# Kernel tuning notes

Hardware: AMD Instinct MI355X
Metric: run time of the kernel (lower is better)

Reference implementation:

```python
import jax, jax.numpy as jnp
import numpy as np

N = 100_000
E = 1_000_000
F_IN = 128
F_OUT = 64
NHOP = 2


def _xavier(k, shape, gain=1.414):
    fan_in, fan_out = shape
    std = gain * np.sqrt(2.0 / (fan_in + fan_out))
    return (jax.random.normal(k, shape) * std).astype(jnp.float32)


def setup_inputs() -> dict:
    key = jax.random.key(0)
    ks = jax.random.split(key, 8)
    x = jax.random.normal(ks[0], (N, F_IN), jnp.float32)
    edge_index = jax.random.randint(ks[1], (2, E), 0, N)
    edge_attr = jax.random.uniform(ks[2], (E,), jnp.float32)
    W0 = _xavier(ks[3], (F_IN, F_OUT))
    W1 = _xavier(ks[4], (F_IN, F_OUT))
    b0 = jnp.zeros((F_OUT,), jnp.float32)
    b1 = jnp.zeros((F_OUT,), jnp.float32)
    fc0 = _xavier(ks[5], (F_OUT, 1))
    fc1 = _xavier(ks[6], (F_OUT, 1))
    bf0 = jnp.zeros((1,), jnp.float32)
    bf1 = jnp.zeros((1,), jnp.float32)
    return dict(x=x, edge_index=edge_index, edge_attr=edge_attr,
                W0=W0, b0=b0, W1=W1, b1=b1,
                fc0=fc0, bf0=bf0, fc1=fc1, bf1=bf1)


def _spmm(row, col, val, v, n):
    # (A v)[r] = sum over edges (r -> c) of val * v[c]
    return jax.ops.segment_sum(val[:, None] * v[col], row, num_segments=n)


def _adaptive_enc(y, fc, bf):
    # NodeAdaptiveEncoder (eval mode): relu(y) + sigmoid(y@fc+bf) * min(y, 0)
    g = jax.nn.sigmoid(y @ fc + bf)  # [N, 1]
    return jnp.where(y < 0, 0.0, y) + g * jnp.where(y > 0, 0.0, y)


def reference(x, edge_index, edge_attr, W0, b0, W1, b1, fc0, bf0, fc1, bf1):
    n = x.shape[0]
    row, col = edge_index[0], edge_index[1]
    ones = jnp.ones((n, 1), x.dtype)
    params = [(W0, b0, fc0, bf0), (W1, b1, fc1, bf1)]
    outs = []
    for hop in range(NHOP):
        W, b, fc, bf = params[hop]
        h = x @ W  # [N, F_OUT]
        # identity attention; row_uniform norm of A^(hop+1) factors as
        # (A^(hop+1) h) / (A^(hop+1) 1) -- exact since spspmm sums duplicates.
        agg, deg = h, ones
        for _ in range(hop + 1):
            agg = _spmm(row, col, edge_attr, agg, n)
            deg = _spmm(row, col, edge_attr, deg, n)
        safe_deg = jnp.where(deg > 0, deg, 1.0)
        y = jnp.where(deg > 0, agg / safe_deg, 0.0)  # NaN mask for empty rows
        y = y + b
        outs.append(_adaptive_enc(y, fc, bf))
    return jnp.concatenate(outs, axis=1)  # [N, NHOP * F_OUT]
```

## Files before the change

kernel.cpp:

```cpp
#include <hip/hip_runtime.h>

#define F_IN 128
#define F_ALL 128
#define F_HOP 64

#define RPB_BITS 9
#define RPB 512
#define KB_MAX 256
#define NBLK_BIN 256
#define BCAP 16

typedef unsigned int uint;
typedef unsigned short ushort;
typedef __attribute__((ext_vector_type(8))) short short8v;
typedef __attribute__((ext_vector_type(4))) float float4v;

__device__ __forceinline__ uint pack_bf16(float lo, float hi) {
    uint ul = __float_as_uint(lo), uh = __float_as_uint(hi);
    ul += 0x7FFFu + ((ul >> 16) & 1u);
    uh += 0x7FFFu + ((uh >> 16) & 1u);
    return (ul >> 16) | (uh & 0xFFFF0000u);
}
__device__ __forceinline__ float bf_lo(uint h) { return __uint_as_float(h << 16); }
__device__ __forceinline__ float bf_hi(uint h) { return __uint_as_float(h & 0xFFFF0000u); }
__device__ __forceinline__ ushort to_bf16(float x) {
    uint u = __float_as_uint(x);
    u += 0x7FFFu + ((u >> 16) & 1u);
    return (ushort)(u >> 16);
}

__global__ __launch_bounds__(256) void gemm_mfma_kernel(
    const float* __restrict__ x, const float* __restrict__ W0,
    const float* __restrict__ W1, uint* __restrict__ H2, int N) {
    __shared__ ushort Wlds[16384];

    {
        const int t = threadIdx.x;
        #pragma unroll
        for (int i = 0; i < 8; ++i) {
            const int e    = t + 256 * i;
            const int lane = e & 63;
            const int tile = e >> 6;
            const int kt   = tile >> 3;
            const int nt   = tile & 7;
            const int k0   = kt * 32 + (lane >> 4) * 8;
            const int n    = nt * 16 + (lane & 15);
            const float* src = (n < 64) ? (W0 + n) : (W1 + (n - 64));
            float v[8];
            #pragma unroll
            for (int j = 0; j < 8; ++j) v[j] = src[(size_t)(k0 + j) * F_HOP];
            uint4 o;
            o.x = pack_bf16(v[0], v[1]);
            o.y = pack_bf16(v[2], v[3]);
            o.z = pack_bf16(v[4], v[5]);
            o.w = pack_bf16(v[6], v[7]);
            *((uint4*)Wlds + e) = o;
        }
    }
    __syncthreads();

    const int wv   = threadIdx.x >> 6;
    const int lane = threadIdx.x & 63;
    const int rbase = blockIdx.x * 64 + wv * 16;
    if (rbase >= N) return;

    const int m    = lane & 15;
    const int quad = lane >> 4;
    const float* xrow = x + (size_t)(rbase + m) * F_IN + quad * 8;

    float4v acc[8];
    #pragma unroll
    for (int t = 0; t < 8; ++t) acc[t] = (float4v){0.f, 0.f, 0.f, 0.f};

    #pragma unroll
    for (int kt = 0; kt < 4; ++kt) {
        const float4 xa = *(const float4*)(xrow + kt * 32);
        const float4 xb = *(const float4*)(xrow + kt * 32 + 4);
        union { uint4 u; short8v s; } av;
        av.u.x = pack_bf16(xa.x, xa.y);
        av.u.y = pack_bf16(xa.z, xa.w);
        av.u.z = pack_bf16(xb.x, xb.y);
        av.u.w = pack_bf16(xb.z, xb.w);
        #pragma unroll
        for (int nt = 0; nt < 8; ++nt) {
            union { uint4 u; short8v s; } bv;
            bv.u = *((const uint4*)Wlds + (kt * 8 + nt) * 64 + lane);
            acc[nt] = __builtin_amdgcn_mfma_f32_16x16x32_bf16(av.s, bv.s, acc[nt], 0, 0, 0);
        }
    }

    #pragma unroll
    for (int t = 0; t < 4; ++t) {
        #pragma unroll
        for (int i = 0; i < 4; ++i) {
            const int r = rbase + quad * 4 + i;
            H2[(size_t)r * F_HOP + t * 16 + m] = pack_bf16(acc[t][i], acc[t + 4][i]);
        }
    }
}

__global__ __launch_bounds__(256) void bucket_hist_kernel(
    const int* __restrict__ ei, int* __restrict__ bhist, int E, int K) {
    __shared__ int h[KB_MAX];
    for (int i = threadIdx.x; i < K; i += 256) h[i] = 0;
    __syncthreads();
    const int chunk = (E + NBLK_BIN - 1) / NBLK_BIN;
    const int s = blockIdx.x * chunk;
    const int e = min(s + chunk, E);
    for (int j = s + threadIdx.x; j < e; j += 256)
        atomicAdd(&h[ei[j] >> RPB_BITS], 1);
    __syncthreads();
    for (int i = threadIdx.x; i < K; i += 256)
        bhist[blockIdx.x * KB_MAX + i] = h[i];
}

__global__ __launch_bounds__(256) void bucket_scan_kernel(
    int* __restrict__ bhist, int* __restrict__ bbase,
    int* __restrict__ rowptr, int E, int K, int N) {
    __shared__ int wsum[4];
    const int t = threadIdx.x;
    int s = 0;
    if (t < K)
        for (int i = 0; i < NBLK_BIN; ++i) s += bhist[i * KB_MAX + t];
    int v = s;
    #pragma unroll
    for (int d = 1; d < 64; d <<= 1) {
        int u = __shfl_up(v, (unsigned)d, 64);
        if ((t & 63) >= d) v += u;
    }
    if ((t & 63) == 63) wsum[t >> 6] = v;
    __syncthreads();
    int off = 0;
    #pragma unroll
    for (int i = 0; i < 4; ++i) if (i < (t >> 6)) off += wsum[i];
    const int excl = off + v - s;
    if (t < K) {
        bbase[t] = excl;
        int run = excl;
        for (int i = 0; i < NBLK_BIN; ++i) {
            const int idx = i * KB_MAX + t;
            const int c = bhist[idx];
            bhist[idx] = run;
            run += c;
        }
    }
    if (t == 0) { bbase[K] = E; rowptr[N] = E; }
}

__global__ __launch_bounds__(256) void bin_kernel(
    const int* __restrict__ ei, const float* __restrict__ ea,
    const int* __restrict__ bloc, int2* __restrict__ gbuf, int E, int K) {
    __shared__ int buf[KB_MAX * (2 * BCAP + 1)];
    __shared__ int lcnt[KB_MAX];
    __shared__ int cur[KB_MAX];
    for (int i = threadIdx.x; i < K; i += 256) {
        lcnt[i] = 0;
        cur[i] = bloc[blockIdx.x * KB_MAX + i];
    }
    __syncthreads();
    const int chunk = (E + NBLK_BIN - 1) / NBLK_BIN;
    const int s0 = blockIdx.x * chunk;
    const int e0 = min(s0 + chunk, E);
    for (int base = s0; base < e0; base += 256) {
        const int j = base + threadIdx.x;
        if (j < e0) {
            const int r = ei[j];
            const int c = ei[E + j];
            const int vv = __float_as_int(ea[j]);
            const int b = r >> RPB_BITS;
            const int w0 = c | ((r & (RPB - 1)) << 17);
            const int pos = atomicAdd(&lcnt[b], 1);
            if (pos < BCAP) {
                const int boff = b * (2 * BCAP + 1) + 2 * pos;
                buf[boff] = w0; buf[boff + 1] = vv;
            } else {
                const int gp = atomicAdd(&cur[b], 1);
                gbuf[gp] = make_int2(w0, vv);
            }
        }
        __syncthreads();
        for (int b = threadIdx.x; b < K; b += 256) {
            int c = lcnt[b]; if (c > BCAP) c = BCAP;
            if (c >= 8) {
                const int n = c & ~7;
                const int gp = cur[b]; cur[b] = gp + n;
                const int boff = b * (2 * BCAP + 1);
                for (int i = 0; i < n; ++i)
                    gbuf[gp + i] = make_int2(buf[boff + 2 * i], buf[boff + 2 * i + 1]);
                for (int i = n; i < c; ++i) {
                    buf[boff + 2 * (i - n)]     = buf[boff + 2 * i];
                    buf[boff + 2 * (i - n) + 1] = buf[boff + 2 * i + 1];
                }
                lcnt[b] = c - n;
            } else {
                lcnt[b] = c;
            }
        }
        __syncthreads();
    }
    for (int b = threadIdx.x; b < K; b += 256) {
        int c = lcnt[b]; if (c > BCAP) c = BCAP;
        if (c > 0) {
            const int gp = cur[b];
            const int boff = b * (2 * BCAP + 1);
            for (int i = 0; i < c; ++i)
                gbuf[gp + i] = make_int2(buf[boff + 2 * i], buf[boff + 2 * i + 1]);
        }
    }
}

__global__ __launch_bounds__(256) void sort_kernel(
    const int* __restrict__ bbase, const int2* __restrict__ gbuf,
    int2* __restrict__ ecv, int* __restrict__ rowptr, int N) {
    __shared__ int cnt[RPB];
    __shared__ int nxt[RPB];
    __shared__ int wsum[4];
    const int b = blockIdx.x;
    const int t = threadIdx.x;
    const int bstart = bbase[b], bend = bbase[b + 1];
    const int row0 = b << RPB_BITS;
    for (int i = t; i < RPB; i += 256) cnt[i] = 0;
    __syncthreads();
    for (int j = bstart + t; j < bend; j += 256)
        atomicAdd(&cnt[(gbuf[j].x >> 17) & (RPB - 1)], 1);
    __syncthreads();
    const int c0 = cnt[2 * t], c1 = cnt[2 * t + 1];
    const int s = c0 + c1;
    int v = s;
    #pragma unroll
    for (int d = 1; d < 64; d <<= 1) {
        int u = __shfl_up(v, (unsigned)d, 64);
        if ((t & 63) >= d) v += u;
    }
    if ((t & 63) == 63) wsum[t >> 6] = v;
    __syncthreads();
    int off = 0;
    #pragma unroll
    for (int i = 0; i < 4; ++i) if (i < (t >> 6)) off += wsum[i];
    const int e0 = off + v - s;
    nxt[2 * t]     = e0;
    nxt[2 * t + 1] = e0 + c0;
    const int r0 = row0 + 2 * t, r1 = row0 + 2 * t + 1;
    if (r0 < N) rowptr[r0] = bstart + e0;
    if (r1 < N) rowptr[r1] = bstart + e0 + c0;
    __syncthreads();
    for (int j = bstart + t; j < bend; j += 256) {
        const int2 p = gbuf[j];
        const int lr = (p.x >> 17) & (RPB - 1);
        const int pos = atomicAdd(&nxt[lr], 1);
        ecv[bstart + pos] = make_int2(p.x & 0x1FFFF, p.y);
    }
}

__global__ __launch_bounds__(256) void pass1_kernel(
    const int* __restrict__ rowptr, const int2* __restrict__ ecv,
    const uint* __restrict__ H2,
    const float* __restrict__ b0, const float* __restrict__ fc0,
    const float* __restrict__ bf0,
    float* __restrict__ out, ushort* __restrict__ T16,
    float* __restrict__ dg1, int N) {
    const int lane = threadIdx.x & 63;
    const int g    = lane >> 4;
    const int l    = lane & 15;
    const int r = blockIdx.x * 16 + (threadIdx.x >> 6) * 4 + g;
    if (r >= N) return;
    const int f0 = l * 4;
    const uint* __restrict__ H2b = H2 + f0;
    const int jb = rowptr[r], je = rowptr[r + 1];

    float s00 = 0.f, s01 = 0.f, s02 = 0.f, s03 = 0.f;
    float s10 = 0.f, s11 = 0.f, s12 = 0.f, s13 = 0.f;
    float d = 0.f;
    int j = jb;
    for (; j + 4 <= je; j += 4) {
        const int2 e0 = ecv[j], e1 = ecv[j + 1], e2 = ecv[j + 2], e3 = ecv[j + 3];
        const uint4 h0 = *(const uint4*)(H2b + (size_t)e0.x * F_HOP);
        const uint4 h1 = *(const uint4*)(H2b + (size_t)e1.x * F_HOP);
        const uint4 h2 = *(const uint4*)(H2b + (size_t)e2.x * F_HOP);
        const uint4 h3 = *(const uint4*)(H2b + (size_t)e3.x * F_HOP);
        const float v0 = __int_as_float(e0.y), v1 = __int_as_float(e1.y);
        const float v2 = __int_as_float(e2.y), v3 = __int_as_float(e3.y);
        d += (v0 + v1) + (v2 + v3);
        s00 = fmaf(v0, bf_lo(h0.x), s00); s10 = fmaf(v0, bf_hi(h0.x), s10);
        s01 = fmaf(v0, bf_lo(h0.y), s01); s11 = fmaf(v0, bf_hi(h0.y), s11);
        s02 = fmaf(v0, bf_lo(h0.z), s02); s12 = fmaf(v0, bf_hi(h0.z), s12);
        s03 = fmaf(v0, bf_lo(h0.w), s03); s13 = fmaf(v0, bf_hi(h0.w), s13);
        s00 = fmaf(v1, bf_lo(h1.x), s00); s10 = fmaf(v1, bf_hi(h1.x), s10);
        s01 = fmaf(v1, bf_lo(h1.y), s01); s11 = fmaf(v1, bf_hi(h1.y), s11);
        s02 = fmaf(v1, bf_lo(h1.z), s02); s12 = fmaf(v1, bf_hi(h1.z), s12);
        s03 = fmaf(v1, bf_lo(h1.w), s03); s13 = fmaf(v1, bf_hi(h1.w), s13);
        s00 = fmaf(v2, bf_lo(h2.x), s00); s10 = fmaf(v2, bf_hi(h2.x), s10);
        s01 = fmaf(v2, bf_lo(h2.y), s01); s11 = fmaf(v2, bf_hi(h2.y), s11);
        s02 = fmaf(v2, bf_lo(h2.z), s02); s12 = fmaf(v2, bf_hi(h2.z), s12);
        s03 = fmaf(v2, bf_lo(h2.w), s03); s13 = fmaf(v2, bf_hi(h2.w), s13);
        s00 = fmaf(v3, bf_lo(h3.x), s00); s10 = fmaf(v3, bf_hi(h3.x), s10);
        s01 = fmaf(v3, bf_lo(h3.y), s01); s11 = fmaf(v3, bf_hi(h3.y), s11);
        s02 = fmaf(v3, bf_lo(h3.z), s02); s12 = fmaf(v3, bf_hi(h3.z), s12);
        s03 = fmaf(v3, bf_lo(h3.w), s03); s13 = fmaf(v3, bf_hi(h3.w), s13);
    }
    for (; j < je; ++j) {
        const int2 e0 = ecv[j];
        const uint4 h0 = *(const uint4*)(H2b + (size_t)e0.x * F_HOP);
        const float v0 = __int_as_float(e0.y);
        d += v0;
        s00 = fmaf(v0, bf_lo(h0.x), s00); s10 = fmaf(v0, bf_hi(h0.x), s10);
        s01 = fmaf(v0, bf_lo(h0.y), s01); s11 = fmaf(v0, bf_hi(h0.y), s11);
        s02 = fmaf(v0, bf_lo(h0.z), s02); s12 = fmaf(v0, bf_hi(h0.z), s12);
        s03 = fmaf(v0, bf_lo(h0.w), s03); s13 = fmaf(v0, bf_hi(h0.w), s13);
    }

    uint2 tw;
    tw.x = pack_bf16(s10, s11);
    tw.y = pack_bf16(s12, s13);
    *(uint2*)(T16 + (size_t)r * F_HOP + f0) = tw;
    if (l == 0) dg1[r] = d;

    const float inv = (d > 0.f) ? 1.f / d : 0.f;
    const float4 bb = *(const float4*)(b0 + f0);
    const float4 ff = *(const float4*)(fc0 + f0);
    const float y0 = s00 * inv + bb.x;
    const float y1 = s01 * inv + bb.y;
    const float y2 = s02 * inv + bb.z;
    const float y3 = s03 * inv + bb.w;
    float t = y0 * ff.x + y1 * ff.y + y2 * ff.z + y3 * ff.w;
    #pragma unroll
    for (int m = 1; m < 16; m <<= 1) t += __shfl_xor(t, m, 64);
    const float gg = 1.f / (1.f + __expf(-(t + bf0[0])));
    float4 o;
    o.x = fmaxf(y0, 0.f) + gg * fminf(y0, 0.f);
    o.y = fmaxf(y1, 0.f) + gg * fminf(y1, 0.f);
    o.z = fmaxf(y2, 0.f) + gg * fminf(y2, 0.f);
    o.w = fmaxf(y3, 0.f) + gg * fminf(y3, 0.f);
    *(float4*)(out + (size_t)r * F_ALL + f0) = o;
}

__global__ __launch_bounds__(256) void pass2_kernel(
    const int* __restrict__ rowptr, const int2* __restrict__ ecv,
    const ushort* __restrict__ T16, const float* __restrict__ dg1,
    const float* __restrict__ b1, const float* __restrict__ fc1,
    const float* __restrict__ bf1,
    float* __restrict__ out, int N) {
    const int lane = threadIdx.x & 63;
    const int g    = lane >> 4;
    const int l    = lane & 15;
    const int r = blockIdx.x * 16 + (threadIdx.x >> 6) * 4 + g;
    if (r >= N) return;
    const int f0 = l * 4;
    const ushort* __restrict__ Tb = T16 + f0;
    const int jb = rowptr[r], je = rowptr[r + 1];

    float s0 = 0.f, s1 = 0.f, s2 = 0.f, s3 = 0.f;
    float d2 = 0.f;
    int j = jb;
    for (; j + 4 <= je; j += 4) {
        const int2 e0 = ecv[j], e1 = ecv[j + 1], e2 = ecv[j + 2], e3 = ecv[j + 3];
        const uint2 t0 = *(const uint2*)(Tb + (size_t)e0.x * F_HOP);
        const uint2 t1 = *(const uint2*)(Tb + (size_t)e1.x * F_HOP);
        const uint2 t2 = *(const uint2*)(Tb + (size_t)e2.x * F_HOP);
        const uint2 t3 = *(const uint2*)(Tb + (size_t)e3.x * F_HOP);
        const float g0 = dg1[e0.x], g1 = dg1[e1.x], g2 = dg1[e2.x], g3 = dg1[e3.x];
        const float v0 = __int_as_float(e0.y), v1 = __int_as_float(e1.y);
        const float v2 = __int_as_float(e2.y), v3 = __int_as_float(e3.y);
        d2 = fmaf(v0, g0, d2); d2 = fmaf(v1, g1, d2);
        d2 = fmaf(v2, g2, d2); d2 = fmaf(v3, g3, d2);
        s0 = fmaf(v0, bf_lo(t0.x), s0); s1 = fmaf(v0, bf_hi(t0.x), s1);
        s2 = fmaf(v0, bf_lo(t0.y), s2); s3 = fmaf(v0, bf_hi(t0.y), s3);
        s0 = fmaf(v1, bf_lo(t1.x), s0); s1 = fmaf(v1, bf_hi(t1.x), s1);
        s2 = fmaf(v1, bf_lo(t1.y), s2); s3 = fmaf(v1, bf_hi(t1.y), s3);
        s0 = fmaf(v2, bf_lo(t2.x), s0); s1 = fmaf(v2, bf_hi(t2.x), s1);
        s2 = fmaf(v2, bf_lo(t2.y), s2); s3 = fmaf(v2, bf_hi(t2.y), s3);
        s0 = fmaf(v3, bf_lo(t3.x), s0); s1 = fmaf(v3, bf_hi(t3.x), s1);
        s2 = fmaf(v3, bf_lo(t3.y), s2); s3 = fmaf(v3, bf_hi(t3.y), s3);
    }
    for (; j < je; ++j) {
        const int2 e0 = ecv[j];
        const uint2 t0 = *(const uint2*)(Tb + (size_t)e0.x * F_HOP);
        const float v0 = __int_as_float(e0.y);
        d2 = fmaf(v0, dg1[e0.x], d2);
        s0 = fmaf(v0, bf_lo(t0.x), s0); s1 = fmaf(v0, bf_hi(t0.x), s1);
        s2 = fmaf(v0, bf_lo(t0.y), s2); s3 = fmaf(v0, bf_hi(t0.y), s3);
    }

    const float inv = (d2 > 0.f) ? 1.f / d2 : 0.f;
    const float4 bb = *(const float4*)(b1 + f0);
    const float4 ff = *(const float4*)(fc1 + f0);
    const float y0 = s0 * inv + bb.x;
    const float y1 = s1 * inv + bb.y;
    const float y2 = s2 * inv + bb.z;
    const float y3 = s3 * inv + bb.w;
    float t = y0 * ff.x + y1 * ff.y + y2 * ff.z + y3 * ff.w;
    #pragma unroll
    for (int m = 1; m < 16; m <<= 1) t += __shfl_xor(t, m, 64);
    const float gg = 1.f / (1.f + __expf(-(t + bf1[0])));
    float4 o;
    o.x = fmaxf(y0, 0.f) + gg * fminf(y0, 0.f);
    o.y = fmaxf(y1, 0.f) + gg * fminf(y1, 0.f);
    o.z = fmaxf(y2, 0.f) + gg * fminf(y2, 0.f);
    o.w = fmaxf(y3, 0.f) + gg * fminf(y3, 0.f);
    *(float4*)(out + (size_t)r * F_ALL + F_HOP + f0) = o;
}

extern "C" void kernel_launch(void* const* d_in, const int* in_sizes, int n_in,
                              void* d_out, int out_size, void* d_ws, size_t ws_size,
                              hipStream_t stream) {
    const float* x   = (const float*)d_in[0];
    const int*   ei  = (const int*)  d_in[1];
    const float* ea  = (const float*)d_in[2];
    const float* W0  = (const float*)d_in[3];
    const float* b0  = (const float*)d_in[4];
    const float* W1  = (const float*)d_in[5];
    const float* b1  = (const float*)d_in[6];
    const float* fc0 = (const float*)d_in[7];
    const float* bf0 = (const float*)d_in[8];
    const float* fc1 = (const float*)d_in[9];
    const float* bf1 = (const float*)d_in[10];
    float* out = (float*)d_out;

    const int N = in_sizes[0] / F_IN;
    const int E = in_sizes[2];
    const int K = (N + RPB - 1) >> RPB_BITS;

    uint*   H2   = (uint*)d_ws;
    ushort* T16  = (ushort*)(H2 + (size_t)N * F_HOP);
    float*  dg1  = (float*)(T16 + (size_t)N * F_HOP);
    int2*   gbuf = (int2*)(dg1 + (size_t)((N + 3) & ~3));
    int2*   ecv  = gbuf + (size_t)E;
    int*    bhist = (int*)(ecv + (size_t)E);
    int*    bbase = bhist + (size_t)NBLK_BIN * KB_MAX;
    int*    rowptr = bbase + (KB_MAX + 8);

    gemm_mfma_kernel<<<(N + 63) / 64, 256, 0, stream>>>(x, W0, W1, H2, N);

    bucket_hist_kernel<<<NBLK_BIN, 256, 0, stream>>>(ei, bhist, E, K);
    bucket_scan_kernel<<<1, 256, 0, stream>>>(bhist, bbase, rowptr, E, K, N);
    bin_kernel<<<NBLK_BIN, 256, 0, stream>>>(ei, ea, bhist, gbuf, E, K);
    sort_kernel<<<K, 256, 0, stream>>>(bbase, gbuf, ecv, rowptr, N);

    pass1_kernel<<<(N + 15) / 16, 256, 0, stream>>>(
        rowptr, ecv, H2, b0, fc0, bf0, out, T16, dg1, N);

    pass2_kernel<<<(N + 15) / 16, 256, 0, stream>>>(
        rowptr, ecv, T16, dg1, b1, fc1, bf1, out, N);
}
```

Measured before the change: 258.3 us.

## Parallelize bucket scan, simplify binning, stage bucket edges in LDS during sort

Replaces the single-block serial bucket scan with a per-bucket parallel block scan followed by a small total scan. The binning kernel drops its LDS staging buffers and writes each edge straight to global memory via a shared-memory cursor atomic. The sort kernel now runs 512 threads, one per row in the bucket, and caches up to ECAP edges in LDS so the second pass avoids re-reading global memory. This targets the serial scan latency and the heavy synchronisation in binning, at the cost of less coalesced scatter writes and a large LDS footprint in sort that may limit occupancy.

After: 235.5 us. 1.1x faster.

```diff
diff --git a/kernel.cpp b/kernel.cpp
--- a/kernel.cpp
+++ b/kernel.cpp
@@ -8,7 +8,7 @@
 #define RPB 512
 #define KB_MAX 256
 #define NBLK_BIN 256
-#define BCAP 16
+#define ECAP 6144
 
 typedef unsigned int uint;
 typedef unsigned short ushort;
@@ -23,11 +23,6 @@
 }
 __device__ __forceinline__ float bf_lo(uint h) { return __uint_as_float(h << 16); }
 __device__ __forceinline__ float bf_hi(uint h) { return __uint_as_float(h & 0xFFFF0000u); }
-__device__ __forceinline__ ushort to_bf16(float x) {
-    uint u = __float_as_uint(x);
-    u += 0x7FFFu + ((u >> 16) & 1u);
-    return (ushort)(u >> 16);
-}
 
 __global__ __launch_bounds__(256) void gemm_mfma_kernel(
     const float* __restrict__ x, const float* __restrict__ W0,
@@ -114,14 +109,33 @@
         bhist[blockIdx.x * KB_MAX + i] = h[i];
 }
 
-__global__ __launch_bounds__(256) void bucket_scan_kernel(
-    int* __restrict__ bhist, int* __restrict__ bbase,
+__global__ __launch_bounds__(256) void blockscan_kernel(
+    int* __restrict__ bhist, int* __restrict__ btot) {
+    __shared__ int wsum[4];
+    const int b = blockIdx.x;
+    const int t = threadIdx.x;
+    const int s = bhist[t * KB_MAX + b];
+    int v = s;
+    #pragma unroll
+    for (int d = 1; d < 64; d <<= 1) {
+        int u = __shfl_up(v, (unsigned)d, 64);
+        if ((t & 63) >= d) v += u;
+    }
+    if ((t & 63) == 63) wsum[t >> 6] = v;
+    __syncthreads();
+    int off = 0;
+    #pragma unroll
+    for (int i = 0; i < 4; ++i) if (i < (t >> 6)) off += wsum[i];
+    bhist[t * KB_MAX + b] = off + v - s;
+    if (t == 255) btot[b] = off + v;
+}
+
+__global__ __launch_bounds__(256) void total_scan_kernel(
+    const int* __restrict__ btot, int* __restrict__ bbase,
     int* __restrict__ rowptr, int E, int K, int N) {
     __shared__ int wsum[4];
     const int t = threadIdx.x;
-    int s = 0;
-    if (t < K)
-        for (int i = 0; i < NBLK_BIN; ++i) s += bhist[i * KB_MAX + t];
+    const int s = (t < K) ? btot[t] : 0;
     int v = s;
     #pragma unroll
     for (int d = 1; d < 64; d <<= 1) {
@@ -134,98 +148,51 @@
     #pragma unroll
     for (int i = 0; i < 4; ++i) if (i < (t >> 6)) off += wsum[i];
     const int excl = off + v - s;
-    if (t < K) {
-        bbase[t] = excl;
-        int run = excl;
-        for (int i = 0; i < NBLK_BIN; ++i) {
-            const int idx = i * KB_MAX + t;
-            const int c = bhist[idx];
-            bhist[idx] = run;
-            run += c;
-        }
-    }
+    if (t < K) bbase[t] = excl;
     if (t == 0) { bbase[K] = E; rowptr[N] = E; }
 }
 
 __global__ __launch_bounds__(256) void bin_kernel(
     const int* __restrict__ ei, const float* __restrict__ ea,
-    const int* __restrict__ bloc, int2* __restrict__ gbuf, int E, int K) {
-    __shared__ int buf[KB_MAX * (2 * BCAP + 1)];
-    __shared__ int lcnt[KB_MAX];
+    const int* __restrict__ bloc, const int* __restrict__ bbase,
+    int2* __restrict__ gbuf, int E, int K) {
     __shared__ int cur[KB_MAX];
-    for (int i = threadIdx.x; i < K; i += 256) {
-        lcnt[i] = 0;
-        cur[i] = bloc[blockIdx.x * KB_MAX + i];
-    }
+    for (int i = threadIdx.x; i < K; i += 256)
+        cur[i] = bbase[i] + bloc[blockIdx.x * KB_MAX + i];
     __syncthreads();
     const int chunk = (E + NBLK_BIN - 1) / NBLK_BIN;
     const int s0 = blockIdx.x * chunk;
     const int e0 = min(s0 + chunk, E);
-    for (int base = s0; base < e0; base += 256) {
-        const int j = base + threadIdx.x;
-        if (j < e0) {
-            const int r = ei[j];
-            const int c = ei[E + j];
-            const int vv = __float_as_int(ea[j]);
-            const int b = r >> RPB_BITS;
-            const int w0 = c | ((r & (RPB - 1)) << 17);
-            const int pos = atomicAdd(&lcnt[b], 1);
-            if (pos < BCAP) {
-                const int boff = b * (2 * BCAP + 1) + 2 * pos;
-                buf[boff] = w0; buf[boff + 1] = vv;
-            } else {
-                const int gp = atomicAdd(&cur[b], 1);
-                gbuf[gp] = make_int2(w0, vv);
-            }
-        }
-        __syncthreads();
-        for (int b = threadIdx.x; b < K; b += 256) {
-            int c = lcnt[b]; if (c > BCAP) c = BCAP;
-            if (c >= 8) {
-                const int n = c & ~7;
-                const int gp = cur[b]; cur[b] = gp + n;
-                const int boff = b * (2 * BCAP + 1);
-                for (int i = 0; i < n; ++i)
-                    gbuf[gp + i] = make_int2(buf[boff + 2 * i], buf[boff + 2 * i + 1]);
-                for (int i = n; i < c; ++i) {
-                    buf[boff + 2 * (i - n)]     = buf[boff + 2 * i];
-                    buf[boff + 2 * (i - n) + 1] = buf[boff + 2 * i + 1];
-                }
-                lcnt[b] = c - n;
-            } else {
-                lcnt[b] = c;
-            }
-        }
-        __syncthreads();
-    }
-    for (int b = threadIdx.x; b < K; b += 256) {
-        int c = lcnt[b]; if (c > BCAP) c = BCAP;
-        if (c > 0) {
-            const int gp = cur[b];
-            const int boff = b * (2 * BCAP + 1);
-            for (int i = 0; i < c; ++i)
-                gbuf[gp + i] = make_int2(buf[boff + 2 * i], buf[boff + 2 * i + 1]);
-        }
-    }
-}
-
-__global__ __launch_bounds__(256) void sort_kernel(
+    for (int j = s0 + threadIdx.x; j < e0; j += 256) {
+        const int r = ei[j];
+        const int c = ei[E + j];
+        const int vv = __float_as_int(ea[j]);
+        const int b = r >> RPB_BITS;
+        const int gp = atomicAdd(&cur[b], 1);
+        gbuf[gp] = make_int2(c | ((r & (RPB - 1)) << 17), vv);
+    }
+}
+
+__global__ __launch_bounds__(512) void sort_kernel(
     const int* __restrict__ bbase, const int2* __restrict__ gbuf,
     int2* __restrict__ ecv, int* __restrict__ rowptr, int N) {
+    __shared__ int2 ebuf[ECAP];
     __shared__ int cnt[RPB];
-    __shared__ int nxt[RPB];
-    __shared__ int wsum[4];
+    __shared__ int wsum[8];
     const int b = blockIdx.x;
     const int t = threadIdx.x;
     const int bstart = bbase[b], bend = bbase[b + 1];
+    const int m = bend - bstart;
     const int row0 = b << RPB_BITS;
-    for (int i = t; i < RPB; i += 256) cnt[i] = 0;
-    __syncthreads();
-    for (int j = bstart + t; j < bend; j += 256)
-        atomicAdd(&cnt[(gbuf[j].x >> 17) & (RPB - 1)], 1);
-    __syncthreads();
-    const int c0 = cnt[2 * t], c1 = cnt[2 * t + 1];
-    const int s = c0 + c1;
+    cnt[t] = 0;
+    __syncthreads();
+    for (int j = t; j < m; j += 512) {
+        const int2 p = gbuf[bstart + j];
+        if (j < ECAP) ebuf[j] = p;
+        atomicAdd(&cnt[(p.x >> 17) & (RPB - 1)], 1);
+    }
+    __syncthreads();
+    const int s = cnt[t];
     int v = s;
     #pragma unroll
     for (int d = 1; d < 64; d <<= 1) {
@@ -236,18 +203,17 @@
     __syncthreads();
     int off = 0;
     #pragma unroll
-    for (int i = 0; i < 4; ++i) if (i < (t >> 6)) off += wsum[i];
-    const int e0 = off + v - s;
-    nxt[2 * t]     = e0;
-    nxt[2 * t + 1] = e0 + c0;
-    const int r0 = row0 + 2 * t, r1 = row0 + 2 * t + 1;
-    if (r0 < N) rowptr[r0] = bstart + e0;
-    if (r1 < N) rowptr[r1] = bstart + e0 + c0;
-    __syncthreads();
-    for (int j = bstart + t; j < bend; j += 256) {
-        const int2 p = gbuf[j];
+    for (int i = 0; i < 8; ++i) if (i < (t >> 6)) off += wsum[i];
+    const int excl = off + v - s;
+    const int r0 = row0 + t;
+    if (r0 < N) rowptr[r0] = bstart + excl;
+    __syncthreads();
+    cnt[t] = excl;
+    __syncthreads();
+    for (int j = t; j < m; j += 512) {
+        const int2 p = (j < ECAP) ? ebuf[j] : gbuf[bstart + j];
         const int lr = (p.x >> 17) & (RPB - 1);
-        const int pos = atomicAdd(&nxt[lr], 1);
+        const int pos = atomicAdd(&cnt[lr], 1);
         ecv[bstart + pos] = make_int2(p.x & 0x1FFFF, p.y);
     }
 }
@@ -427,14 +393,16 @@
     int2*   ecv  = gbuf + (size_t)E;
     int*    bhist = (int*)(ecv + (size_t)E);
     int*    bbase = bhist + (size_t)NBLK_BIN * KB_MAX;
-    int*    rowptr = bbase + (KB_MAX + 8);
+    int*    btot  = bbase + (KB_MAX + 4);
+    int*    rowptr = btot + KB_MAX;
 
     gemm_mfma_kernel<<<(N + 63) / 64, 256, 0, stream>>>(x, W0, W1, H2, N);
 
     bucket_hist_kernel<<<NBLK_BIN, 256, 0, stream>>>(ei, bhist, E, K);
-    bucket_scan_kernel<<<1, 256, 0, stream>>>(bhist, bbase, rowptr, E, K, N);
-    bin_kernel<<<NBLK_BIN, 256, 0, stream>>>(ei, ea, bhist, gbuf, E, K);
-    sort_kernel<<<K, 256, 0, stream>>>(bbase, gbuf, ecv, rowptr, N);
+    blockscan_kernel<<<K, 256, 0, stream>>>(bhist, btot);
+    total_scan_kernel<<<1, 256, 0, stream>>>(btot, bbase, rowptr, E, K, N);
+    bin_kernel<<<NBLK_BIN, 256, 0, stream>>>(ei, ea, bhist, bbase, gbuf, E, K);
+    sort_kernel<<<K, 512, 0, stream>>>(bbase, gbuf, ecv, rowptr, N);
 
     pass1_kernel<<<(N + 15) / 16, 256, 0, stream>>>(
         rowptr, ecv, H2, b0, fc0, bf0, out, T16, dg1, N);
```
